# Optimization experiments

Hardware: AMD Instinct MI355X
Metric: run time of the kernel (lower is better)

## Reference

```python
import jax, jax.numpy as jnp
import numpy as np

U, B, S, R = 64, 256, 256, 512
N = 4096
EMA_DECAY = 0.99


def setup_inputs() -> dict:
    key = jax.random.key(0)
    ks = jax.random.split(key, 9)
    q_u = jax.random.uniform(ks[0], (N, U), dtype=jnp.float32)
    q_b = jax.random.uniform(ks[1], (N, B), dtype=jnp.float32)
    q_sigma = jax.random.normal(ks[2], (N, S), dtype=jnp.float32)
    delta_rule_target = jax.random.normal(ks[3], (N, R), dtype=jnp.float32)
    write_mask = jax.random.randint(ks[4], (N,), 0, 2).astype(bool)
    delta_rule_proto = 0.02 * jax.random.normal(ks[5], (U, B, R), dtype=jnp.float32)
    signature_proto = 0.02 * jax.random.normal(ks[6], (U, B, S), dtype=jnp.float32)
    ema_conf = jax.random.uniform(ks[7], (U, B), dtype=jnp.float32)
    usage_count = jnp.maximum(jax.random.uniform(ks[8], (U, B)) - 0.5, 0.0) * 100.0
    return {"q_u": q_u, "q_b": q_b, "q_sigma": q_sigma,
            "delta_rule_target": delta_rule_target, "write_mask": write_mask,
            "delta_rule_proto": delta_rule_proto, "signature_proto": signature_proto,
            "ema_conf": ema_conf, "usage_count": usage_count}


def _l2norm(x):
    return x / jnp.maximum(jnp.linalg.norm(x, axis=-1, keepdims=True), 1e-12)


def reference(q_u, q_b, q_sigma, delta_rule_target, write_mask,
              delta_rule_proto, signature_proto, ema_conf, usage_count):
    # ---------------- retrieve ----------------
    # joint attention over (operator, binding) cells; temperature == 1.0 branch
    joint = q_u[:, :, None] * q_b[:, None, :]                  # [N, U, B]
    valid = (usage_count > 0).astype(joint.dtype)              # [U, B]
    w = joint * valid
    denom = w.sum(axis=(-2, -1), keepdims=True)
    w = jnp.where(denom > 0, w / jnp.maximum(denom, 1e-6), jnp.zeros_like(w))
    memory_delta_rule = jnp.einsum('nub,ubr->nr', w, delta_rule_proto)
    memory_signature = jnp.einsum('nub,ubs->ns', w, signature_proto)
    base_conf = jnp.einsum('nub,ub->n', w, ema_conf)[:, None]  # [N, 1]
    cos = jnp.sum(_l2norm(q_sigma) * _l2norm(memory_signature + 1e-6),
                  axis=-1, keepdims=True)
    signature_agreement = 0.5 * (1.0 + cos)
    memory_conf = jnp.clip(base_conf * signature_agreement, 0.0, 1.0)

    # ---------------- update (vectorized scatter EMA) ----------------
    m = write_mask.astype(q_u.dtype)                           # [N]
    op_conf = q_u.max(axis=-1)
    op_id = jnp.argmax(q_u, axis=-1)
    bind_conf = q_b.max(axis=-1)
    bind_id = jnp.argmax(q_b, axis=-1)
    write_conf = op_conf * bind_conf                           # [N]
    cell = op_id * B + bind_id                                 # [N]
    num_cells = U * B
    wgt = write_conf * m
    sum_w = jax.ops.segment_sum(wgt, cell, num_segments=num_cells)          # [UB]
    sum_d = jax.ops.segment_sum(delta_rule_target * wgt[:, None], cell,
                                num_segments=num_cells)                     # [UB, R]
    sum_s = jax.ops.segment_sum(q_sigma * wgt[:, None], cell,
                                num_segments=num_cells)                     # [UB, S]
    cnt = jax.ops.segment_sum(m, cell, num_segments=num_cells)              # [UB]
    conf_sum = jnp.maximum(sum_w, 1e-6)
    delta_mean = (sum_d / conf_sum[:, None]).reshape(U, B, R)
    sigma_mean = (sum_s / conf_sum[:, None]).reshape(U, B, S)
    conf_mean = (sum_w / jnp.maximum(cnt, 1.0)).reshape(U, B)
    upd = (cnt > 0).reshape(U, B)
    new_delta_proto = jnp.where(upd[:, :, None],
                                EMA_DECAY * delta_rule_proto + (1.0 - EMA_DECAY) * delta_mean,
                                delta_rule_proto)
    new_signature_proto = jnp.where(upd[:, :, None],
                                    EMA_DECAY * signature_proto + (1.0 - EMA_DECAY) * sigma_mean,
                                    signature_proto)
    new_ema_conf = jnp.where(upd,
                             EMA_DECAY * ema_conf + (1.0 - EMA_DECAY) * conf_mean,
                             ema_conf)
    new_usage = usage_count + cnt.reshape(U, B)

    # ---------------- usage stats ----------------
    write_rate = m.mean()
    usage_fraction = (new_usage > 0).astype(jnp.float32).mean()
    dist = new_usage.reshape(-1)
    dist = dist / jnp.maximum(dist.sum(), 1e-6)
    usage_entropy = -(dist * jnp.log(dist + 1e-6)).sum() / np.log(max(2, num_cells))

    return (memory_delta_rule, memory_signature, memory_conf,
            new_delta_proto, new_signature_proto, new_ema_conf, new_usage,
            write_rate, usage_fraction, usage_entropy)
```

## Files before the change

kernel.cpp:

```cpp
#include <hip/hip_runtime.h>
#include <hip/hip_fp8.h>
#include <math.h>

#define NR 4096
#define UD 64
#define BD 256
#define SD 256
#define RD 512
#define UBD 16384
#define DECAY 0.99f

typedef unsigned char u8;
typedef __attribute__((ext_vector_type(4))) float f32x4;
typedef __attribute__((ext_vector_type(2))) long longx2;

#define OFF_MDR   0ull
#define OFF_MSIG  2097152ull
#define OFF_MCONF 3145728ull
#define OFF_NDP   3149824ull
#define OFF_NSP   11538432ull
#define OFF_NEC   15732736ull
#define OFF_NUS   15749120ull
#define OFF_SCAL  15765504ull

static __device__ __forceinline__ u8 f2e4m3(float x) {
  __hip_fp8_e4m3 h(x);
  return (u8)h.__x;
}

static __device__ __forceinline__ void gll16(const void* g, void* l) {
  __builtin_amdgcn_global_load_lds(
      (const __attribute__((address_space(1))) unsigned int*)g,
      (__attribute__((address_space(3))) unsigned int*)l, 16, 0, 0);
}

static __device__ __forceinline__ int perm64(int x) {
  return (((x >> 3) & 3) << 4) | (((x >> 5) & 1) << 3) | (x & 7);
}

__global__ __launch_bounds__(256) void row_prep_kernel(
    const float* __restrict__ q_u, const float* __restrict__ q_b,
    const float* __restrict__ usage, const float* __restrict__ ema,
    const unsigned char* __restrict__ wm,
    float* __restrict__ denom, float* __restrict__ base_raw,
    float* __restrict__ wgt, int* __restrict__ cellid, float* __restrict__ mrow,
    float* __restrict__ sum_w, float* __restrict__ cnt)
{
  const int r0 = blockIdx.x * 16;
  const int t = threadIdx.x;
  __shared__ float s_qu[16][64];
  __shared__ float s_qbv[16][256];
  __shared__ float s_pd[16][256];
  __shared__ float s_pc[16][256];
  __shared__ int s_flag;
  {
    const float4 v = *(const float4*)(q_u + (size_t)r0 * UD + t * 4);
    float* dst = &s_qu[0][0] + t * 4;
    dst[0] = v.x; dst[1] = v.y; dst[2] = v.z; dst[3] = v.w;
  }
  {
    const float4* src = (const float4*)(q_b + (size_t)r0 * BD);
    float4* dst = (float4*)&s_qbv[0][0];
    #pragma unroll
    for (int i = 0; i < 4; ++i) dst[t + i * 256] = src[t + i * 256];
  }
  if (t == 0) {
    const int*   wi = (const int*)wm;
    const float* wf = (const float*)wm;
    bool is_i32 = true, is_f32 = true;
    #pragma unroll
    for (int i = 0; i < 16; ++i) {
      int v = wi[i];
      if (v != 0 && v != 1) is_i32 = false;
      float f = wf[i];
      if (f != 0.f && f != 1.f) is_f32 = false;
    }
    s_flag = is_i32 ? 2 : (is_f32 ? 1 : 0);
  }
  __syncthreads();
  float accd[16], accc[16];
  #pragma unroll
  for (int r = 0; r < 16; ++r) { accd[r] = 0.f; accc[r] = 0.f; }
  #pragma unroll 2
  for (int u = 0; u < UD; ++u) {
    const float us = usage[u * BD + t];
    const float em = ema[u * BD + t];
    const float vm = (us > 0.f) ? 1.f : 0.f;
    const float ev = em * vm;
    #pragma unroll
    for (int r = 0; r < 16; ++r) {
      accd[r] += s_qu[r][u] * vm;
      accc[r] += s_qu[r][u] * ev;
    }
  }
  #pragma unroll
  for (int r = 0; r < 16; ++r) {
    s_pd[r][t] = accd[r] * s_qbv[r][t];
    s_pc[r][t] = accc[r] * s_qbv[r][t];
  }
  __syncthreads();
  const int w = t >> 6, l = t & 63;
  #pragma unroll
  for (int rr = 0; rr < 4; ++rr) {
    const int row = w * 4 + rr;
    float dsum = s_pd[row][l] + s_pd[row][l + 64] + s_pd[row][l + 128] + s_pd[row][l + 192];
    float csum = s_pc[row][l] + s_pc[row][l + 64] + s_pc[row][l + 128] + s_pc[row][l + 192];
    #pragma unroll
    for (int m = 1; m < 64; m <<= 1) {
      dsum += __shfl_xor(dsum, m);
      csum += __shfl_xor(csum, m);
    }
    float bv_ = s_qbv[row][l]; int bi_ = l;
    #pragma unroll
    for (int k = 1; k < 4; ++k) {
      const float v2 = s_qbv[row][l + k * 64];
      if (v2 > bv_) { bv_ = v2; bi_ = l + k * 64; }
    }
    #pragma unroll
    for (int m = 1; m < 64; m <<= 1) {
      const float ov = __shfl_xor(bv_, m);
      const int   oi = __shfl_xor(bi_, m);
      if (ov > bv_ || (ov == bv_ && oi < bi_)) { bv_ = ov; bi_ = oi; }
    }
    float uv_ = s_qu[row][l]; int ui_ = l;
    #pragma unroll
    for (int m = 1; m < 64; m <<= 1) {
      const float ov = __shfl_xor(uv_, m);
      const int   oi = __shfl_xor(ui_, m);
      if (ov > uv_ || (ov == uv_ && oi < ui_)) { uv_ = ov; ui_ = oi; }
    }
    if (l == 0) {
      const int n = r0 + row;
      const int fm = s_flag;
      float m;
      if (fm == 2)      m = (((const int*)wm)[n]   != 0)   ? 1.f : 0.f;
      else if (fm == 1) m = (((const float*)wm)[n] != 0.f) ? 1.f : 0.f;
      else              m = (wm[n] != 0)   ? 1.f : 0.f;
      const float wv = uv_ * bv_ * m;
      const int cell = ui_ * BD + bi_;
      denom[n]    = dsum;
      base_raw[n] = csum;
      wgt[n]      = wv;
      cellid[n]   = cell;
      mrow[n]     = m;
      if (m != 0.f) {
        atomicAdd(&sum_w[cell], wv);
        atomicAdd(&cnt[cell], 1.f);
      }
    }
  }
}

__global__ __launch_bounds__(256) void prep_kernel(
    const float* __restrict__ qb, const float* __restrict__ qu,
    u8* __restrict__ qb8, float* __restrict__ quT)
{
  if (blockIdx.x < 1024) {
    const int i = blockIdx.x * 256 + threadIdx.x;
    const int idx = i * 4;
    const int row = idx >> 8;
    const int b   = idx & 255;
    const float4 v = *(const float4*)(qb + (size_t)idx);
    u8 tmp[4] = { f2e4m3(v.x), f2e4m3(v.y), f2e4m3(v.z), f2e4m3(v.w) };
    unsigned int wv; __builtin_memcpy(&wv, tmp, 4);
    const int nb = (b & ~63) | perm64(b & 63);
    *(unsigned int*)(qb8 + (size_t)row * BD + nb) = wv;
  } else {
    __shared__ float s[64][65];
    const int n0 = (blockIdx.x - 1024) * 64;
    const int tid = threadIdx.x;
    #pragma unroll
    for (int i = 0; i < 16; ++i) {
      const int idx = tid + i * 256;
      const int r = idx >> 6, u = idx & 63;
      s[r][u] = qu[(size_t)(n0 + r) * UD + u];
    }
    __syncthreads();
    #pragma unroll
    for (int i = 0; i < 16; ++i) {
      const int idx = tid + i * 256;
      const int u = idx >> 6, r = idx & 63;
      quT[(size_t)u * NR + n0 + r] = s[r][u];
    }
  }
}

__global__ __launch_bounds__(256) void transpose_mask_kernel(
    const float* __restrict__ dproto, const float* __restrict__ sproto,
    const float* __restrict__ usage, u8* __restrict__ PT8)
{
  __shared__ u8 s[64][68];
  const int k0 = blockIdx.x * 64;
  const int rblk = blockIdx.y;
  const float* src; int ld; int c0s;
  if (rblk < 8) { src = dproto; ld = RD; c0s = rblk * 64; }
  else          { src = sproto; ld = SD; c0s = (rblk - 8) * 64; }
  const int tid = threadIdx.x;
  const int kl = tid >> 4;
  const int rl = (tid & 15) * 4;
  #pragma unroll
  for (int i = 0; i < 4; ++i) {
    const int k = kl + i * 16;
    const bool valid = usage[k0 + k] > 0.f;
    const float4 v = *(const float4*)(src + (size_t)(k0 + k) * ld + c0s + rl);
    s[k][rl + 0] = valid ? f2e4m3(v.x) : (u8)0;
    s[k][rl + 1] = valid ? f2e4m3(v.y) : (u8)0;
    s[k][rl + 2] = valid ? f2e4m3(v.z) : (u8)0;
    s[k][rl + 3] = valid ? f2e4m3(v.w) : (u8)0;
  }
  __syncthreads();
  const int rl2 = tid >> 4;
  const int kl2 = (tid & 15) * 4;
  #pragma unroll
  for (int i = 0; i < 4; ++i) {
    const int r = rl2 + i * 16;
    u8 tmp[4] = { s[kl2 + 0][r], s[kl2 + 1][r], s[kl2 + 2][r], s[kl2 + 3][r] };
    unsigned int wv; __builtin_memcpy(&wv, tmp, 4);
    *(unsigned int*)(PT8 + (size_t)(rblk * 64 + r) * UBD + k0 + perm64(kl2)) = wv;
  }
}

__global__ __launch_bounds__(256, 3) void mfma_gemm_kernel(
    const float* __restrict__ quT, const u8* __restrict__ qb8,
    const u8* __restrict__ PT8, float* __restrict__ out,
    int* __restrict__ tk, int* __restrict__ gf, int* __restrict__ claimed)
{
  __shared__ u8 sA[2][128 * 128];
  __shared__ u8 sB[2][128 * 64];
  __shared__ int s_work;
  const int tid = threadIdx.x;

  if (tid == 0) {
    unsigned int xcc;
    asm volatile("s_getreg_b32 %0, hwreg(HW_REG_XCC_ID)" : "=s"(xcc));
    const int x = (int)(xcc & 7u);
    const int t = atomicAdd(&tk[x], 1);
    int w = -1;
    if (t < 96) {
      const int cand = x * 96 + t;
      if (atomicCAS(&claimed[cand], 0, 1) == 0) w = cand;
    }
    while (w < 0) {
      const int g = atomicAdd(gf, 1);
      if (g >= 768) { w = -2; break; }
      if (atomicCAS(&claimed[g], 0, 1) == 0) w = g;
    }
    s_work = w;
  }
  __syncthreads();
  const int w = s_work;
  if (w < 0) return;

  const int bx = w & 31;
  const int combo = w >> 5;
  const int by = combo >> 2;
  const int bz = combo & 3;

  const int wid = tid >> 6, lane = tid & 63;
  const int n0 = bx * 128;
  const int kbeg = bz * (UBD / 4);

  float* obase; int ldO; int cc0;
  if (by < 4) { obase = out + OFF_MDR;  ldO = RD; cc0 = by * 128; }
  else        { obase = out + OFF_MSIG; ldO = SD; cc0 = (by - 4) * 128; }
  const int c0 = by * 128;

  const int lrowA = lane >> 3;
  const int csrcA = ((lane & 7) ^ lrowA) * 16;
  const u8* gA = qb8 + (size_t)(n0 + lrowA) * BD + csrcA;
  const int lrowB = lane >> 2;
  const int srcslotB = (lane & 3) ^ ((lrowB >> 1) & 3);
  const u8* gB = PT8 + (size_t)(c0 + wid * 16 + lrowB) * UBD + kbeg + srcslotB * 16;

  const int wr = (wid >> 1) * 64, wc = (wid & 1) * 64;
  const int fr = lane & 15;
  const int kg = lane >> 4;
  int aoff[4], boff[4];
  #pragma unroll
  for (int m = 0; m < 4; ++m) aoff[m] = (wr + m * 16 + fr) * 128;
  #pragma unroll
  for (int nn = 0; nn < 4; ++nn) boff[nn] = (wc + nn * 16 + fr) * 64;
  int slothA[2];
  #pragma unroll
  for (int bq = 0; bq < 2; ++bq) slothA[bq] = ((bq * 4 + kg) ^ (fr & 7)) * 16;
  const int slotB16 = (kg ^ ((fr >> 1) & 3)) * 16;

  f32x4 accm[4][4];
  #pragma unroll
  for (int m = 0; m < 4; ++m)
    #pragma unroll
    for (int nn = 0; nn < 4; ++nn)
      accm[m][nn] = (f32x4){0.f, 0.f, 0.f, 0.f};

  #pragma unroll
  for (int i = 0; i < 4; ++i) {
    const int ro = wid * 32 + i * 8;
    gll16(gA + (size_t)ro * BD,       &sA[0][ro * 128]);
    gll16(gA + (size_t)ro * BD + 128, &sA[1][ro * 128]);
  }
  #pragma unroll
  for (int i = 0; i < 2; ++i)
    gll16(gB + (size_t)(i * 64) * UBD, &sB[0][(i * 64 + wid * 16) * 64]);
  __syncthreads();

  const float* quTb = quT + n0 + wr + kg * 4;
  const int ubase = kbeg >> 8;
  f32x4 accu[4][4];

  for (int ph = 0; ph < 64; ++ph) {
    const int buf  = ph & 1;
    const int half = (ph >> 1) & 1;
    const int bq   = ph & 1;
    if (ph < 63) {
      const u8* gs = gB + (size_t)(ph + 1) * 64;
      #pragma unroll
      for (int i = 0; i < 2; ++i)
        gll16(gs + (size_t)(i * 64) * UBD, &sB[buf ^ 1][(i * 64 + wid * 16) * 64]);
    }
    const u8* sa = sA[half];
    const u8* sb = sB[buf];
    longx2 av[4], bv[4];
    #pragma unroll
    for (int m = 0; m < 4; ++m)
      av[m] = *(const longx2*)(sa + aoff[m] + slothA[bq]);
    #pragma unroll
    for (int nn = 0; nn < 4; ++nn)
      bv[nn] = *(const longx2*)(sb + boff[nn] + slotB16);
    const bool first = (ph & 3) == 0;
    #pragma unroll
    for (int m = 0; m < 4; ++m)
      #pragma unroll
      for (int nn = 0; nn < 4; ++nn) {
        if (first)
          accu[m][nn] = __builtin_amdgcn_mfma_f32_16x16x32_fp8_fp8(
              av[m].x, bv[nn].x, (f32x4){0.f, 0.f, 0.f, 0.f}, 0, 0, 0);
        else
          accu[m][nn] = __builtin_amdgcn_mfma_f32_16x16x32_fp8_fp8(
              av[m].x, bv[nn].x, accu[m][nn], 0, 0, 0);
        accu[m][nn] = __builtin_amdgcn_mfma_f32_16x16x32_fp8_fp8(
            av[m].y, bv[nn].y, accu[m][nn], 0, 0, 0);
      }
    __syncthreads();
    if ((ph & 3) == 3) {
      const float* qp = quTb + (size_t)(ubase + (ph >> 2)) * NR;
      #pragma unroll
      for (int m = 0; m < 4; ++m) {
        const f32x4 qv = *(const f32x4*)(qp + m * 16);
        #pragma unroll
        for (int nn = 0; nn < 4; ++nn)
          accm[m][nn] += qv * accu[m][nn];
      }
    }
  }

  #pragma unroll
  for (int m = 0; m < 4; ++m) {
    #pragma unroll
    for (int nn = 0; nn < 4; ++nn) {
      const int c = cc0 + wc + nn * 16 + fr;
      #pragma unroll
      for (int j = 0; j < 4; ++j) {
        const int r = n0 + wr + m * 16 + kg * 4 + j;
        atomicAdd(obase + (size_t)r * ldO + c, accm[m][nn][j]);
      }
    }
  }
}

__global__ __launch_bounds__(256) void epilogue_kernel(
    const float* __restrict__ q_sigma, const float* __restrict__ denom,
    const float* __restrict__ base_raw, float* __restrict__ out)
{
  const int n = blockIdx.x;
  const int t = threadIdx.x;
  __shared__ float r1[256], r2[256], r3[256];
  const float d = denom[n];
  const float scale = (d > 0.f) ? (1.f / fmaxf(d, 1e-6f)) : 0.f;
  float* mdr = out + OFF_MDR + (size_t)n * RD;
  mdr[t]       *= scale;
  mdr[t + 256] *= scale;
  float* msig = out + OFF_MSIG + (size_t)n * SD;
  const float s = msig[t] * scale;
  msig[t] = s;
  const float a = q_sigma[(size_t)n * SD + t];
  const float b = s + 1e-6f;
  r1[t] = a * a; r2[t] = b * b; r3[t] = a * b;
  __syncthreads();
  for (int st = 128; st > 0; st >>= 1) {
    if (t < st) { r1[t] += r1[t + st]; r2[t] += r2[t + st]; r3[t] += r3[t + st]; }
    __syncthreads();
  }
  if (t == 0) {
    const float na = fmaxf(sqrtf(r1[0]), 1e-12f);
    const float nb = fmaxf(sqrtf(r2[0]), 1e-12f);
    const float cosv = r3[0] / (na * nb);
    const float agree = 0.5f * (1.f + cosv);
    const float base = (d > 0.f) ? base_raw[n] / fmaxf(d, 1e-6f) : 0.f;
    out[OFF_MCONF + n] = fminf(fmaxf(base * agree, 0.f), 1.f);
  }
}

__global__ __launch_bounds__(256) void ema_copy_kernel(
    const float* __restrict__ dproto, const float* __restrict__ sproto,
    const float* __restrict__ cnt,
    float* __restrict__ outd, float* __restrict__ outs)
{
  const size_t nd = (size_t)UBD * RD;
  const size_t total = nd + (size_t)UBD * SD;
  for (size_t i = (size_t)blockIdx.x * 256 + threadIdx.x; i < total;
       i += (size_t)gridDim.x * 256) {
    if (i < nd) {
      const float p = dproto[i];
      outd[i] = (cnt[(int)(i >> 9)] > 0.f) ? DECAY * p : p;
    } else {
      const size_t j = i - nd;
      const float p = sproto[j];
      outs[j] = (cnt[(int)(j >> 8)] > 0.f) ? DECAY * p : p;
    }
  }
}

__global__ __launch_bounds__(256) void scatter2_kernel(
    const float* __restrict__ dtarget, const float* __restrict__ q_sigma,
    const float* __restrict__ wgt, const int* __restrict__ cellid,
    const float* __restrict__ mrow, const float* __restrict__ sum_w,
    float* __restrict__ outd, float* __restrict__ outs)
{
  const int n = blockIdx.x;
  if (mrow[n] == 0.f) return;
  const int t = threadIdx.x;
  const int c = cellid[n];
  const float cs = fmaxf(sum_w[c], 1e-6f);
  const float coef = (1.0f - DECAY) * wgt[n] / cs;
  atomicAdd(&outd[(size_t)c * RD + t],       dtarget[(size_t)n * RD + t] * coef);
  atomicAdd(&outd[(size_t)c * RD + t + 256], dtarget[(size_t)n * RD + t + 256] * coef);
  atomicAdd(&outs[(size_t)c * SD + t],       q_sigma[(size_t)n * SD + t] * coef);
}

__global__ __launch_bounds__(256) void ema_small_kernel(
    const float* __restrict__ ema, const float* __restrict__ usage,
    const float* __restrict__ sum_w, const float* __restrict__ cnt,
    float* __restrict__ out_ec, float* __restrict__ out_us)
{
  const int i = blockIdx.x * 256 + threadIdx.x;
  if (i < UBD) {
    const float c = cnt[i];
    const float cm = sum_w[i] / fmaxf(c, 1.f);
    out_ec[i] = (c > 0.f) ? DECAY * ema[i] + (1.f - DECAY) * cm : ema[i];
    out_us[i] = usage[i] + c;
  }
}

__global__ __launch_bounds__(256) void stats_kernel(
    const float* __restrict__ cnt, const float* __restrict__ new_us,
    float* __restrict__ out_scalars)
{
  const int t = threadIdx.x;
  __shared__ float r1[256], r2[256], r3[256];
  float scnt = 0.f, snz = 0.f, sus = 0.f;
  for (int i = t; i < UBD; i += 256) {
    const float c = cnt[i]; scnt += c;
    const float u = new_us[i];
    if (u > 0.f) snz += 1.f;
    sus += u;
  }
  r1[t] = scnt; r2[t] = snz; r3[t] = sus;
  __syncthreads();
  for (int s = 128; s > 0; s >>= 1) {
    if (t < s) { r1[t] += r1[t + s]; r2[t] += r2[t + s]; r3[t] += r3[t + s]; }
    __syncthreads();
  }
  const float total_cnt = r1[0], total_nz = r2[0], total_us = r3[0];
  __syncthreads();
  const float S = fmaxf(total_us, 1e-6f);
  float ent = 0.f;
  for (int i = t; i < UBD; i += 256) {
    const float d = new_us[i] / S;
    ent += d * logf(d + 1e-6f);
  }
  r1[t] = ent;
  __syncthreads();
  for (int s = 128; s > 0; s >>= 1) {
    if (t < s) { r1[t] += r1[t + s]; }
    __syncthreads();
  }
  if (t == 0) {
    out_scalars[0] = total_cnt / (float)NR;
    out_scalars[1] = total_nz / (float)UBD;
    out_scalars[2] = -r1[0] / 9.70406053f;
  }
}

extern "C" void kernel_launch(void* const* d_in, const int* in_sizes, int n_in,
                              void* d_out, int out_size, void* d_ws, size_t ws_size,
                              hipStream_t stream)
{
  const float* q_u    = (const float*)d_in[0];
  const float* q_b    = (const float*)d_in[1];
  const float* q_sig  = (const float*)d_in[2];
  const float* dtg    = (const float*)d_in[3];
  const unsigned char* wm = (const unsigned char*)d_in[4];
  const float* dproto = (const float*)d_in[5];
  const float* sproto = (const float*)d_in[6];
  const float* ema    = (const float*)d_in[7];
  const float* usage  = (const float*)d_in[8];
  float* out = (float*)d_out;

  float* wsf = (float*)d_ws;
  int*   wsi = (int*)d_ws;
  float* denom    = wsf + 16;
  float* base_raw = wsf + 16 + 4096;
  float* wgtb     = wsf + 16 + 8192;
  int*   cellid   = wsi + 16 + 12288;
  float* mrow     = wsf + 16 + 16384;
  float* sum_w    = wsf + 20496;
  float* cnt      = wsf + 20496 + 16384;
  int*   tk       = wsi + 53264;
  int*   gf       = wsi + 53272;
  int*   claimed  = wsi + 53280;

  u8*    PT8 = (u8*)(out + OFF_NDP);
  u8*    qb8 = PT8 + (size_t)768 * UBD;
  float* quT = (float*)(qb8 + (size_t)NR * BD);

  prep_kernel<<<1024 + NR / 64, 256, 0, stream>>>(q_b, q_u, qb8, quT);
  transpose_mask_kernel<<<dim3(UBD / 64, 12), 256, 0, stream>>>(dproto, sproto,
                                                                usage, PT8);
  hipMemsetAsync(out, 0, (size_t)OFF_MCONF * sizeof(float), stream);
  hipMemsetAsync(sum_w, 0, (2u * UBD + 16 + 768) * sizeof(float), stream);

  row_prep_kernel<<<NR / 16, 256, 0, stream>>>(q_u, q_b, usage, ema, wm,
                                               denom, base_raw, wgtb, cellid, mrow,
                                               sum_w, cnt);
  mfma_gemm_kernel<<<768, 256, 0, stream>>>(quT, qb8, PT8, out, tk, gf, claimed);
  epilogue_kernel<<<NR, 256, 0, stream>>>(q_sig, denom, base_raw, out);

  ema_copy_kernel<<<4096, 256, 0, stream>>>(dproto, sproto, cnt,
                                            out + OFF_NDP, out + OFF_NSP);
  scatter2_kernel<<<NR, 256, 0, stream>>>(dtg, q_sig, wgtb, cellid, mrow, sum_w,
                                          out + OFF_NDP, out + OFF_NSP);
  ema_small_kernel<<<UBD / 256, 256, 0, stream>>>(ema, usage, sum_w, cnt,
                                                  out + OFF_NEC, out + OFF_NUS);
  stats_kernel<<<1, 256, 0, stream>>>(cnt, out + OFF_NUS, out + OFF_SCAL);
}
```

Measured before the change: 221.7 us.

## Merge prep and post kernels, make GEMM persistent with register-resident A fragments

```diff
diff --git a/kernel.cpp b/kernel.cpp
--- a/kernel.cpp
+++ b/kernel.cpp
@@ -38,142 +38,42 @@
   return (((x >> 3) & 3) << 4) | (((x >> 5) & 1) << 3) | (x & 7);
 }
 
-__global__ __launch_bounds__(256) void row_prep_kernel(
+__global__ __launch_bounds__(256) void prep_all_kernel(
     const float* __restrict__ q_u, const float* __restrict__ q_b,
+    const float* __restrict__ q_sigma_unused,
+    const float* __restrict__ dproto, const float* __restrict__ sproto,
     const float* __restrict__ usage, const float* __restrict__ ema,
     const unsigned char* __restrict__ wm,
+    u8* __restrict__ qb8, float* __restrict__ quT, u8* __restrict__ PT8,
     float* __restrict__ denom, float* __restrict__ base_raw,
     float* __restrict__ wgt, int* __restrict__ cellid, float* __restrict__ mrow,
     float* __restrict__ sum_w, float* __restrict__ cnt)
 {
-  const int r0 = blockIdx.x * 16;
-  const int t = threadIdx.x;
-  __shared__ float s_qu[16][64];
-  __shared__ float s_qbv[16][256];
-  __shared__ float s_pd[16][256];
-  __shared__ float s_pc[16][256];
+  __shared__ __attribute__((aligned(16))) u8 sbuf[53248];
   __shared__ int s_flag;
-  {
-    const float4 v = *(const float4*)(q_u + (size_t)r0 * UD + t * 4);
-    float* dst = &s_qu[0][0] + t * 4;
-    dst[0] = v.x; dst[1] = v.y; dst[2] = v.z; dst[3] = v.w;
-  }
-  {
-    const float4* src = (const float4*)(q_b + (size_t)r0 * BD);
-    float4* dst = (float4*)&s_qbv[0][0];
-    #pragma unroll
-    for (int i = 0; i < 4; ++i) dst[t + i * 256] = src[t + i * 256];
-  }
-  if (t == 0) {
-    const int*   wi = (const int*)wm;
-    const float* wf = (const float*)wm;
-    bool is_i32 = true, is_f32 = true;
-    #pragma unroll
-    for (int i = 0; i < 16; ++i) {
-      int v = wi[i];
-      if (v != 0 && v != 1) is_i32 = false;
-      float f = wf[i];
-      if (f != 0.f && f != 1.f) is_f32 = false;
-    }
-    s_flag = is_i32 ? 2 : (is_f32 ? 1 : 0);
-  }
-  __syncthreads();
-  float accd[16], accc[16];
-  #pragma unroll
-  for (int r = 0; r < 16; ++r) { accd[r] = 0.f; accc[r] = 0.f; }
-  #pragma unroll 2
-  for (int u = 0; u < UD; ++u) {
-    const float us = usage[u * BD + t];
-    const float em = ema[u * BD + t];
-    const float vm = (us > 0.f) ? 1.f : 0.f;
-    const float ev = em * vm;
-    #pragma unroll
-    for (int r = 0; r < 16; ++r) {
-      accd[r] += s_qu[r][u] * vm;
-      accc[r] += s_qu[r][u] * ev;
-    }
-  }
-  #pragma unroll
-  for (int r = 0; r < 16; ++r) {
-    s_pd[r][t] = accd[r] * s_qbv[r][t];
-    s_pc[r][t] = accc[r] * s_qbv[r][t];
-  }
-  __syncthreads();
-  const int w = t >> 6, l = t & 63;
-  #pragma unroll
-  for (int rr = 0; rr < 4; ++rr) {
-    const int row = w * 4 + rr;
-    float dsum = s_pd[row][l] + s_pd[row][l + 64] + s_pd[row][l + 128] + s_pd[row][l + 192];
-    float csum = s_pc[row][l] + s_pc[row][l + 64] + s_pc[row][l + 128] + s_pc[row][l + 192];
-    #pragma unroll
-    for (int m = 1; m < 64; m <<= 1) {
-      dsum += __shfl_xor(dsum, m);
-      csum += __shfl_xor(csum, m);
-    }
-    float bv_ = s_qbv[row][l]; int bi_ = l;
-    #pragma unroll
-    for (int k = 1; k < 4; ++k) {
-      const float v2 = s_qbv[row][l + k * 64];
-      if (v2 > bv_) { bv_ = v2; bi_ = l + k * 64; }
-    }
-    #pragma unroll
-    for (int m = 1; m < 64; m <<= 1) {
-      const float ov = __shfl_xor(bv_, m);
-      const int   oi = __shfl_xor(bi_, m);
-      if (ov > bv_ || (ov == bv_ && oi < bi_)) { bv_ = ov; bi_ = oi; }
-    }
-    float uv_ = s_qu[row][l]; int ui_ = l;
-    #pragma unroll
-    for (int m = 1; m < 64; m <<= 1) {
-      const float ov = __shfl_xor(uv_, m);
-      const int   oi = __shfl_xor(ui_, m);
-      if (ov > uv_ || (ov == uv_ && oi < ui_)) { uv_ = ov; ui_ = oi; }
-    }
-    if (l == 0) {
-      const int n = r0 + row;
-      const int fm = s_flag;
-      float m;
-      if (fm == 2)      m = (((const int*)wm)[n]   != 0)   ? 1.f : 0.f;
-      else if (fm == 1) m = (((const float*)wm)[n] != 0.f) ? 1.f : 0.f;
-      else              m = (wm[n] != 0)   ? 1.f : 0.f;
-      const float wv = uv_ * bv_ * m;
-      const int cell = ui_ * BD + bi_;
-      denom[n]    = dsum;
-      base_raw[n] = csum;
-      wgt[n]      = wv;
-      cellid[n]   = cell;
-      mrow[n]     = m;
-      if (m != 0.f) {
-        atomicAdd(&sum_w[cell], wv);
-        atomicAdd(&cnt[cell], 1.f);
-      }
-    }
-  }
-}
-
-__global__ __launch_bounds__(256) void prep_kernel(
-    const float* __restrict__ qb, const float* __restrict__ qu,
-    u8* __restrict__ qb8, float* __restrict__ quT)
-{
-  if (blockIdx.x < 1024) {
-    const int i = blockIdx.x * 256 + threadIdx.x;
+  const int b = blockIdx.x;
+  const int tid = threadIdx.x;
+
+  if (b < 1024) {
+    const int i = b * 256 + tid;
     const int idx = i * 4;
     const int row = idx >> 8;
-    const int b   = idx & 255;
-    const float4 v = *(const float4*)(qb + (size_t)idx);
+    const int bb  = idx & 255;
+    const float4 v = *(const float4*)(q_b + (size_t)idx);
     u8 tmp[4] = { f2e4m3(v.x), f2e4m3(v.y), f2e4m3(v.z), f2e4m3(v.w) };
     unsigned int wv; __builtin_memcpy(&wv, tmp, 4);
-    const int nb = (b & ~63) | perm64(b & 63);
+    const int nb = (bb & ~63) | perm64(bb & 63);
     *(unsigned int*)(qb8 + (size_t)row * BD + nb) = wv;
-  } else {
-    __shared__ float s[64][65];
-    const int n0 = (blockIdx.x - 1024) * 64;
-    const int tid = threadIdx.x;
+    return;
+  }
+  if (b < 1088) {
+    float (*s)[65] = (float(*)[65])sbuf;
+    const int n0 = (b - 1024) * 64;
     #pragma unroll
     for (int i = 0; i < 16; ++i) {
       const int idx = tid + i * 256;
       const int r = idx >> 6, u = idx & 63;
-      s[r][u] = qu[(size_t)(n0 + r) * UD + u];
+      s[r][u] = q_u[(size_t)(n0 + r) * UD + u];
     }
     __syncthreads();
     #pragma unroll
@@ -182,240 +82,389 @@
       const int u = idx >> 6, r = idx & 63;
       quT[(size_t)u * NR + n0 + r] = s[r][u];
     }
-  }
-}
-
-__global__ __launch_bounds__(256) void transpose_mask_kernel(
-    const float* __restrict__ dproto, const float* __restrict__ sproto,
-    const float* __restrict__ usage, u8* __restrict__ PT8)
-{
-  __shared__ u8 s[64][68];
-  const int k0 = blockIdx.x * 64;
-  const int rblk = blockIdx.y;
-  const float* src; int ld; int c0s;
-  if (rblk < 8) { src = dproto; ld = RD; c0s = rblk * 64; }
-  else          { src = sproto; ld = SD; c0s = (rblk - 8) * 64; }
-  const int tid = threadIdx.x;
-  const int kl = tid >> 4;
-  const int rl = (tid & 15) * 4;
-  #pragma unroll
-  for (int i = 0; i < 4; ++i) {
-    const int k = kl + i * 16;
-    const bool valid = usage[k0 + k] > 0.f;
-    const float4 v = *(const float4*)(src + (size_t)(k0 + k) * ld + c0s + rl);
-    s[k][rl + 0] = valid ? f2e4m3(v.x) : (u8)0;
-    s[k][rl + 1] = valid ? f2e4m3(v.y) : (u8)0;
-    s[k][rl + 2] = valid ? f2e4m3(v.z) : (u8)0;
-    s[k][rl + 3] = valid ? f2e4m3(v.w) : (u8)0;
-  }
-  __syncthreads();
-  const int rl2 = tid >> 4;
-  const int kl2 = (tid & 15) * 4;
-  #pragma unroll
-  for (int i = 0; i < 4; ++i) {
-    const int r = rl2 + i * 16;
-    u8 tmp[4] = { s[kl2 + 0][r], s[kl2 + 1][r], s[kl2 + 2][r], s[kl2 + 3][r] };
-    unsigned int wv; __builtin_memcpy(&wv, tmp, 4);
-    *(unsigned int*)(PT8 + (size_t)(rblk * 64 + r) * UBD + k0 + perm64(kl2)) = wv;
-  }
-}
-
-__global__ __launch_bounds__(256, 3) void mfma_gemm_kernel(
+    return;
+  }
+  if (b < 4160) {
+    u8 (*s)[68] = (u8(*)[68])sbuf;
+    const int idx = b - 1088;
+    const int k0 = (idx & 255) * 64;
+    const int rblk = idx >> 8;
+    const float* src; int ld; int c0s;
+    if (rblk < 8) { src = dproto; ld = RD; c0s = rblk * 64; }
+    else          { src = sproto; ld = SD; c0s = (rblk - 8) * 64; }
+    const int kl = tid >> 4;
+    const int rl = (tid & 15) * 4;
+    #pragma unroll
+    for (int i = 0; i < 4; ++i) {
+      const int k = kl + i * 16;
+      const bool valid = usage[k0 + k] > 0.f;
+      const float4 v = *(const float4*)(src + (size_t)(k0 + k) * ld + c0s + rl);
+      s[k][rl + 0] = valid ? f2e4m3(v.x) : (u8)0;
+      s[k][rl + 1] = valid ? f2e4m3(v.y) : (u8)0;
+      s[k][rl + 2] = valid ? f2e4m3(v.z) : (u8)0;
+      s[k][rl + 3] = valid ? f2e4m3(v.w) : (u8)0;
+    }
+    __syncthreads();
+    const int rl2 = tid >> 4;
+    const int kl2 = (tid & 15) * 4;
+    #pragma unroll
+    for (int i = 0; i < 4; ++i) {
+      const int r = rl2 + i * 16;
+      u8 tmp[4] = { s[kl2 + 0][r], s[kl2 + 1][r], s[kl2 + 2][r], s[kl2 + 3][r] };
+      unsigned int wv; __builtin_memcpy(&wv, tmp, 4);
+      *(unsigned int*)(PT8 + (size_t)(rblk * 64 + r) * UBD + k0 + perm64(kl2)) = wv;
+    }
+    return;
+  }
+  {
+    float (*s_qu)[64]   = (float(*)[64])sbuf;
+    float (*s_qbv)[256] = (float(*)[256])(sbuf + 4096);
+    float (*s_pd)[256]  = (float(*)[256])(sbuf + 20480);
+    float (*s_pc)[256]  = (float(*)[256])(sbuf + 36864);
+    const int r0 = (b - 4160) * 16;
+    {
+      const float4 v = *(const float4*)(q_u + (size_t)r0 * UD + tid * 4);
+      float* dst = &s_qu[0][0] + tid * 4;
+      dst[0] = v.x; dst[1] = v.y; dst[2] = v.z; dst[3] = v.w;
+    }
+    {
+      const float4* src = (const float4*)(q_b + (size_t)r0 * BD);
+      float4* dst = (float4*)&s_qbv[0][0];
+      #pragma unroll
+      for (int i = 0; i < 4; ++i) dst[tid + i * 256] = src[tid + i * 256];
+    }
+    if (tid == 0) {
+      const int*   wi = (const int*)wm;
+      const float* wf = (const float*)wm;
+      bool is_i32 = true, is_f32 = true;
+      #pragma unroll
+      for (int i = 0; i < 16; ++i) {
+        int v = wi[i];
+        if (v != 0 && v != 1) is_i32 = false;
+        float f = wf[i];
+        if (f != 0.f && f != 1.f) is_f32 = false;
+      }
+      s_flag = is_i32 ? 2 : (is_f32 ? 1 : 0);
+    }
+    __syncthreads();
+    float accd[16], accc[16];
+    #pragma unroll
+    for (int r = 0; r < 16; ++r) { accd[r] = 0.f; accc[r] = 0.f; }
+    #pragma unroll 2
+    for (int u = 0; u < UD; ++u) {
+      const float us = usage[u * BD + tid];
+      const float em = ema[u * BD + tid];
+      const float vm = (us > 0.f) ? 1.f : 0.f;
+      const float ev = em * vm;
+      #pragma unroll
+      for (int r = 0; r < 16; ++r) {
+        accd[r] += s_qu[r][u] * vm;
+        accc[r] += s_qu[r][u] * ev;
+      }
+    }
+    #pragma unroll
+    for (int r = 0; r < 16; ++r) {
+      s_pd[r][tid] = accd[r] * s_qbv[r][tid];
+      s_pc[r][tid] = accc[r] * s_qbv[r][tid];
+    }
+    __syncthreads();
+    const int w = tid >> 6, l = tid & 63;
+    #pragma unroll
+    for (int rr = 0; rr < 4; ++rr) {
+      const int row = w * 4 + rr;
+      float dsum = s_pd[row][l] + s_pd[row][l + 64] + s_pd[row][l + 128] + s_pd[row][l + 192];
+      float csum = s_pc[row][l] + s_pc[row][l + 64] + s_pc[row][l + 128] + s_pc[row][l + 192];
+      #pragma unroll
+      for (int m = 1; m < 64; m <<= 1) {
+        dsum += __shfl_xor(dsum, m);
+        csum += __shfl_xor(csum, m);
+      }
+      float bv_ = s_qbv[row][l]; int bi_ = l;
+      #pragma unroll
+      for (int k = 1; k < 4; ++k) {
+        const float v2 = s_qbv[row][l + k * 64];
+        if (v2 > bv_) { bv_ = v2; bi_ = l + k * 64; }
+      }
+      #pragma unroll
+      for (int m = 1; m < 64; m <<= 1) {
+        const float ov = __shfl_xor(bv_, m);
+        const int   oi = __shfl_xor(bi_, m);
+        if (ov > bv_ || (ov == bv_ && oi < bi_)) { bv_ = ov; bi_ = oi; }
+      }
+      float uv_ = s_qu[row][l]; int ui_ = l;
+      #pragma unroll
+      for (int m = 1; m < 64; m <<= 1) {
+        const float ov = __shfl_xor(uv_, m);
+        const int   oi = __shfl_xor(ui_, m);
+        if (ov > uv_ || (ov == uv_ && oi < ui_)) { uv_ = ov; ui_ = oi; }
+      }
+      if (l == 0) {
+        const int n = r0 + row;
+        const int fm = s_flag;
+        float m;
+        if (fm == 2)      m = (((const int*)wm)[n]   != 0)   ? 1.f : 0.f;
+        else if (fm == 1) m = (((const float*)wm)[n] != 0.f) ? 1.f : 0.f;
+        else              m = (wm[n] != 0)   ? 1.f : 0.f;
+        const float wv = uv_ * bv_ * m;
+        const int cell = ui_ * BD + bi_;
+        denom[n]    = dsum;
+        base_raw[n] = csum;
+        wgt[n]      = wv;
+        cellid[n]   = cell;
+        mrow[n]     = m;
+        if (m != 0.f) {
+          atomicAdd(&sum_w[cell], wv);
+          atomicAdd(&cnt[cell], 1.f);
+        }
+      }
+    }
+  }
+}
+
+__global__ __launch_bounds__(256, 2) void mfma_gemm_kernel(
     const float* __restrict__ quT, const u8* __restrict__ qb8,
     const u8* __restrict__ PT8, float* __restrict__ out,
     int* __restrict__ tk, int* __restrict__ gf, int* __restrict__ claimed)
 {
-  __shared__ u8 sA[2][128 * 128];
-  __shared__ u8 sB[2][128 * 64];
+  __shared__ __attribute__((aligned(16))) u8 smB[4 * 2 * 4096];
+  __shared__ __attribute__((aligned(16))) float squT[16 * 128];
   __shared__ int s_work;
   const int tid = threadIdx.x;
-
-  if (tid == 0) {
-    unsigned int xcc;
-    asm volatile("s_getreg_b32 %0, hwreg(HW_REG_XCC_ID)" : "=s"(xcc));
-    const int x = (int)(xcc & 7u);
-    const int t = atomicAdd(&tk[x], 1);
-    int w = -1;
-    if (t < 96) {
-      const int cand = x * 96 + t;
-      if (atomicCAS(&claimed[cand], 0, 1) == 0) w = cand;
-    }
-    while (w < 0) {
-      const int g = atomicAdd(gf, 1);
-      if (g >= 768) { w = -2; break; }
-      if (atomicCAS(&claimed[g], 0, 1) == 0) w = g;
-    }
-    s_work = w;
-  }
-  __syncthreads();
-  const int w = s_work;
-  if (w < 0) return;
-
-  const int bx = w & 31;
-  const int combo = w >> 5;
-  const int by = combo >> 2;
-  const int bz = combo & 3;
-
   const int wid = tid >> 6, lane = tid & 63;
-  const int n0 = bx * 128;
-  const int kbeg = bz * (UBD / 4);
-
-  float* obase; int ldO; int cc0;
-  if (by < 4) { obase = out + OFF_MDR;  ldO = RD; cc0 = by * 128; }
-  else        { obase = out + OFF_MSIG; ldO = SD; cc0 = (by - 4) * 128; }
-  const int c0 = by * 128;
-
-  const int lrowA = lane >> 3;
-  const int csrcA = ((lane & 7) ^ lrowA) * 16;
-  const u8* gA = qb8 + (size_t)(n0 + lrowA) * BD + csrcA;
-  const int lrowB = lane >> 2;
-  const int srcslotB = (lane & 3) ^ ((lrowB >> 1) & 3);
-  const u8* gB = PT8 + (size_t)(c0 + wid * 16 + lrowB) * UBD + kbeg + srcslotB * 16;
 
   const int wr = (wid >> 1) * 64, wc = (wid & 1) * 64;
-  const int fr = lane & 15;
-  const int kg = lane >> 4;
-  int aoff[4], boff[4];
+  const int fr = lane & 15, kg = lane >> 4;
+  const int srow  = lane >> 2;
+  const int sslot = (lane & 3) ^ (srow & 3);
+  u8* myB = smB + wid * 8192;
+  int boff[4];
   #pragma unroll
-  for (int m = 0; m < 4; ++m) aoff[m] = (wr + m * 16 + fr) * 128;
-  #pragma unroll
-  for (int nn = 0; nn < 4; ++nn) boff[nn] = (wc + nn * 16 + fr) * 64;
-  int slothA[2];
-  #pragma unroll
-  for (int bq = 0; bq < 2; ++bq) slothA[bq] = ((bq * 4 + kg) ^ (fr & 7)) * 16;
-  const int slotB16 = (kg ^ ((fr >> 1) & 3)) * 16;
-
-  f32x4 accm[4][4];
-  #pragma unroll
-  for (int m = 0; m < 4; ++m)
-    #pragma unroll
-    for (int nn = 0; nn < 4; ++nn)
-      accm[m][nn] = (f32x4){0.f, 0.f, 0.f, 0.f};
-
-  #pragma unroll
-  for (int i = 0; i < 4; ++i) {
-    const int ro = wid * 32 + i * 8;
-    gll16(gA + (size_t)ro * BD,       &sA[0][ro * 128]);
-    gll16(gA + (size_t)ro * BD + 128, &sA[1][ro * 128]);
-  }
-  #pragma unroll
-  for (int i = 0; i < 2; ++i)
-    gll16(gB + (size_t)(i * 64) * UBD, &sB[0][(i * 64 + wid * 16) * 64]);
-  __syncthreads();
-
-  const float* quTb = quT + n0 + wr + kg * 4;
-  const int ubase = kbeg >> 8;
-  f32x4 accu[4][4];
-
-  for (int ph = 0; ph < 64; ++ph) {
-    const int buf  = ph & 1;
-    const int half = (ph >> 1) & 1;
-    const int bq   = ph & 1;
-    if (ph < 63) {
-      const u8* gs = gB + (size_t)(ph + 1) * 64;
-      #pragma unroll
-      for (int i = 0; i < 2; ++i)
-        gll16(gs + (size_t)(i * 64) * UBD, &sB[buf ^ 1][(i * 64 + wid * 16) * 64]);
-    }
-    const u8* sa = sA[half];
-    const u8* sb = sB[buf];
-    longx2 av[4], bv[4];
+  for (int nn = 0; nn < 4; ++nn)
+    boff[nn] = (nn * 16 + fr) * 64 + ((kg ^ (fr & 3)) << 4);
+
+  for (;;) {
+    if (tid == 0) {
+      unsigned int xcc;
+      asm volatile("s_getreg_b32 %0, hwreg(HW_REG_XCC_ID)" : "=s"(xcc));
+      const int x = (int)(xcc & 7u);
+      const int t = atomicAdd(&tk[x], 1);
+      int w = -1;
+      if (t < 96) {
+        const int cand = x * 96 + t;
+        if (atomicCAS(&claimed[cand], 0, 1) == 0) w = cand;
+      }
+      while (w < 0) {
+        const int g = atomicAdd(gf, 1);
+        if (g >= 768) { w = -2; break; }
+        if (atomicCAS(&claimed[g], 0, 1) == 0) w = g;
+      }
+      s_work = w;
+    }
+    __syncthreads();
+    const int w = s_work;
+    if (w < 0) return;
+
+    const int bx = w & 31;
+    const int combo = w >> 5;
+    const int by = combo >> 2;
+    const int bz = combo & 3;
+    const int n0 = bx * 128;
+    const int kbeg = bz * (UBD / 4);
+    const int ubase = bz * 16;
+    const int c0 = by * 128;
+
+    float* obase; int ldO; int cc0;
+    if (by < 4) { obase = out + OFF_MDR;  ldO = RD; cc0 = by * 128; }
+    else        { obase = out + OFF_MSIG; ldO = SD; cc0 = (by - 4) * 128; }
+
+    longx2 afrag[4][4];
+    {
+      const u8* ga = qb8 + (size_t)(n0 + wr + fr) * BD + kg * 16;
+      #pragma unroll
+      for (int m = 0; m < 4; ++m)
+        #pragma unroll
+        for (int q = 0; q < 4; ++q)
+          afrag[m][q] = *(const longx2*)(ga + (size_t)m * 16 * BD + q * 64);
+    }
+
+    #pragma unroll
+    for (int i = 0; i < 2; ++i) {
+      const int u = wid * 4 + i * 2 + (lane >> 5);
+      const float* src = quT + (size_t)(ubase + u) * NR + n0 + (lane & 31) * 4;
+      gll16(src, (u8*)squT + (wid * 4 + i * 2) * 512);
+    }
+    const u8* gB = PT8 + (size_t)(c0 + wc + srow) * UBD + kbeg + sslot * 16;
+    #pragma unroll
+    for (int c = 0; c < 2; ++c)
+      #pragma unroll
+      for (int j = 0; j < 4; ++j)
+        gll16(gB + (size_t)(j * 16) * UBD + c * 64, myB + c * 4096 + j * 1024);
+    __syncthreads();
+
+    f32x4 accm[4][4], accu[4][4];
     #pragma unroll
     for (int m = 0; m < 4; ++m)
-      av[m] = *(const longx2*)(sa + aoff[m] + slothA[bq]);
-    #pragma unroll
-    for (int nn = 0; nn < 4; ++nn)
-      bv[nn] = *(const longx2*)(sb + boff[nn] + slotB16);
-    const bool first = (ph & 3) == 0;
-    #pragma unroll
-    for (int m = 0; m < 4; ++m)
-      #pragma unroll
-      for (int nn = 0; nn < 4; ++nn) {
-        if (first)
-          accu[m][nn] = __builtin_amdgcn_mfma_f32_16x16x32_fp8_fp8(
-              av[m].x, bv[nn].x, (f32x4){0.f, 0.f, 0.f, 0.f}, 0, 0, 0);
-        else
-          accu[m][nn] = __builtin_amdgcn_mfma_f32_16x16x32_fp8_fp8(
-              av[m].x, bv[nn].x, accu[m][nn], 0, 0, 0);
-        accu[m][nn] = __builtin_amdgcn_mfma_f32_16x16x32_fp8_fp8(
-            av[m].y, bv[nn].y, accu[m][nn], 0, 0, 0);
-      }
-    __syncthreads();
-    if ((ph & 3) == 3) {
-      const float* qp = quTb + (size_t)(ubase + (ph >> 2)) * NR;
-      #pragma unroll
-      for (int m = 0; m < 4; ++m) {
-        const f32x4 qv = *(const f32x4*)(qp + m * 16);
+      #pragma unroll
+      for (int nn = 0; nn < 4; ++nn)
+        accm[m][nn] = (f32x4){0.f, 0.f, 0.f, 0.f};
+
+    for (int uc = 0; uc < 16; ++uc) {
+      #pragma unroll
+      for (int p4 = 0; p4 < 4; ++p4) {
+        const int ph = uc * 4 + p4;
+        if (p4 == 3 && uc == 15) asm volatile("s_waitcnt vmcnt(0)" ::: "memory");
+        else                     asm volatile("s_waitcnt vmcnt(4)" ::: "memory");
+        const u8* sb = myB + (ph & 1) * 4096;
+        longx2 bv[4];
         #pragma unroll
         for (int nn = 0; nn < 4; ++nn)
-          accm[m][nn] += qv * accu[m][nn];
-      }
-    }
-  }
-
-  #pragma unroll
-  for (int m = 0; m < 4; ++m) {
-    #pragma unroll
-    for (int nn = 0; nn < 4; ++nn) {
-      const int c = cc0 + wc + nn * 16 + fr;
-      #pragma unroll
-      for (int j = 0; j < 4; ++j) {
-        const int r = n0 + wr + m * 16 + kg * 4 + j;
-        atomicAdd(obase + (size_t)r * ldO + c, accm[m][nn][j]);
-      }
-    }
-  }
-}
-
-__global__ __launch_bounds__(256) void epilogue_kernel(
+          bv[nn] = *(const longx2*)(sb + boff[nn]);
+        asm volatile("s_waitcnt lgkmcnt(0)" ::: "memory");
+        if (!(uc == 15 && p4 >= 2)) {
+          const u8* gs = gB + (size_t)(ph + 2) * 64;
+          #pragma unroll
+          for (int j = 0; j < 4; ++j)
+            gll16(gs + (size_t)(j * 16) * UBD, myB + (ph & 1) * 4096 + j * 1024);
+        }
+        #pragma unroll
+        for (int m = 0; m < 4; ++m)
+          #pragma unroll
+          for (int nn = 0; nn < 4; ++nn) {
+            if (p4 == 0)
+              accu[m][nn] = __builtin_amdgcn_mfma_f32_16x16x32_fp8_fp8(
+                  afrag[m][p4].x, bv[nn].x, (f32x4){0.f, 0.f, 0.f, 0.f}, 0, 0, 0);
+            else
+              accu[m][nn] = __builtin_amdgcn_mfma_f32_16x16x32_fp8_fp8(
+                  afrag[m][p4].x, bv[nn].x, accu[m][nn], 0, 0, 0);
+            accu[m][nn] = __builtin_amdgcn_mfma_f32_16x16x32_fp8_fp8(
+                afrag[m][p4].y, bv[nn].y, accu[m][nn], 0, 0, 0);
+          }
+        if (p4 == 3) {
+          const float* qs = squT + uc * 128 + wr + kg * 4;
+          #pragma unroll
+          for (int m = 0; m < 4; ++m) {
+            const f32x4 qv = *(const f32x4*)(qs + m * 16);
+            #pragma unroll
+            for (int nn = 0; nn < 4; ++nn)
+              accm[m][nn] += qv * accu[m][nn];
+          }
+        }
+      }
+    }
+
+    #pragma unroll
+    for (int m = 0; m < 4; ++m) {
+      #pragma unroll
+      for (int nn = 0; nn < 4; ++nn) {
+        const int c = cc0 + wc + nn * 16 + fr;
+        #pragma unroll
+        for (int j = 0; j < 4; ++j) {
+          const int r = n0 + wr + m * 16 + kg * 4 + j;
+          atomicAdd(obase + (size_t)r * ldO + c, accm[m][nn][j]);
+        }
+      }
+    }
+  }
+}
+
+__global__ __launch_bounds__(256) void post_all_kernel(
     const float* __restrict__ q_sigma, const float* __restrict__ denom,
-    const float* __restrict__ base_raw, float* __restrict__ out)
+    const float* __restrict__ base_raw,
+    const float* __restrict__ dproto, const float* __restrict__ sproto,
+    const float* __restrict__ ema, const float* __restrict__ usage,
+    const float* __restrict__ sum_w, const float* __restrict__ cnt,
+    float* __restrict__ out)
 {
-  const int n = blockIdx.x;
+  __shared__ float r1[256], r2[256], r3[256];
+  const int b = blockIdx.x;
   const int t = threadIdx.x;
-  __shared__ float r1[256], r2[256], r3[256];
-  const float d = denom[n];
-  const float scale = (d > 0.f) ? (1.f / fmaxf(d, 1e-6f)) : 0.f;
-  float* mdr = out + OFF_MDR + (size_t)n * RD;
-  mdr[t]       *= scale;
-  mdr[t + 256] *= scale;
-  float* msig = out + OFF_MSIG + (size_t)n * SD;
-  const float s = msig[t] * scale;
-  msig[t] = s;
-  const float a = q_sigma[(size_t)n * SD + t];
-  const float b = s + 1e-6f;
-  r1[t] = a * a; r2[t] = b * b; r3[t] = a * b;
-  __syncthreads();
-  for (int st = 128; st > 0; st >>= 1) {
-    if (t < st) { r1[t] += r1[t + st]; r2[t] += r2[t + st]; r3[t] += r3[t + st]; }
-    __syncthreads();
-  }
-  if (t == 0) {
-    const float na = fmaxf(sqrtf(r1[0]), 1e-12f);
-    const float nb = fmaxf(sqrtf(r2[0]), 1e-12f);
-    const float cosv = r3[0] / (na * nb);
-    const float agree = 0.5f * (1.f + cosv);
-    const float base = (d > 0.f) ? base_raw[n] / fmaxf(d, 1e-6f) : 0.f;
-    out[OFF_MCONF + n] = fminf(fmaxf(base * agree, 0.f), 1.f);
-  }
-}
-
-__global__ __launch_bounds__(256) void ema_copy_kernel(
-    const float* __restrict__ dproto, const float* __restrict__ sproto,
-    const float* __restrict__ cnt,
-    float* __restrict__ outd, float* __restrict__ outs)
-{
-  const size_t nd = (size_t)UBD * RD;
-  const size_t total = nd + (size_t)UBD * SD;
-  for (size_t i = (size_t)blockIdx.x * 256 + threadIdx.x; i < total;
-       i += (size_t)gridDim.x * 256) {
-    if (i < nd) {
-      const float p = dproto[i];
-      outd[i] = (cnt[(int)(i >> 9)] > 0.f) ? DECAY * p : p;
-    } else {
-      const size_t j = i - nd;
-      const float p = sproto[j];
-      outs[j] = (cnt[(int)(j >> 8)] > 0.f) ? DECAY * p : p;
+
+  if (b < 4096) {
+    const int n = b;
+    const float d = denom[n];
+    const float scale = (d > 0.f) ? (1.f / fmaxf(d, 1e-6f)) : 0.f;
+    float* mdr = out + OFF_MDR + (size_t)n * RD;
+    mdr[t]       *= scale;
+    mdr[t + 256] *= scale;
+    float* msig = out + OFF_MSIG + (size_t)n * SD;
+    const float s = msig[t] * scale;
+    msig[t] = s;
+    const float a = q_sigma[(size_t)n * SD + t];
+    const float bb = s + 1e-6f;
+    r1[t] = a * a; r2[t] = bb * bb; r3[t] = a * bb;
+    __syncthreads();
+    for (int st = 128; st > 0; st >>= 1) {
+      if (t < st) { r1[t] += r1[t + st]; r2[t] += r2[t + st]; r3[t] += r3[t + st]; }
+      __syncthreads();
+    }
+    if (t == 0) {
+      const float na = fmaxf(sqrtf(r1[0]), 1e-12f);
+      const float nb = fmaxf(sqrtf(r2[0]), 1e-12f);
+      const float cosv = r3[0] / (na * nb);
+      const float agree = 0.5f * (1.f + cosv);
+      const float base = (d > 0.f) ? base_raw[n] / fmaxf(d, 1e-6f) : 0.f;
+      out[OFF_MCONF + n] = fminf(fmaxf(base * agree, 0.f), 1.f);
+    }
+    return;
+  }
+  if (b < 8192) {
+    const size_t nd = (size_t)UBD * RD;
+    const size_t total = nd + (size_t)UBD * SD;
+    float* outd = out + OFF_NDP;
+    float* outs = out + OFF_NSP;
+    for (size_t i = (size_t)(b - 4096) * 256 + t; i < total;
+         i += (size_t)4096 * 256) {
+      if (i < nd) {
+        const float p = dproto[i];
+        outd[i] = (cnt[(int)(i >> 9)] > 0.f) ? DECAY * p : p;
+      } else {
+        const size_t j = i - nd;
+        const float p = sproto[j];
+        outs[j] = (cnt[(int)(j >> 8)] > 0.f) ? DECAY * p : p;
+      }
+    }
+    return;
+  }
+  if (b < 8256) {
+    const int i = (b - 8192) * 256 + t;
+    const float c = cnt[i];
+    const float cm = sum_w[i] / fmaxf(c, 1.f);
+    out[OFF_NEC + i] = (c > 0.f) ? DECAY * ema[i] + (1.f - DECAY) * cm : ema[i];
+    out[OFF_NUS + i] = usage[i] + c;
+    return;
+  }
+  {
+    float scnt = 0.f, snz = 0.f, sus = 0.f;
+    for (int i = t; i < UBD; i += 256) {
+      const float c = cnt[i]; scnt += c;
+      const float u = usage[i] + c;
+      if (u > 0.f) snz += 1.f;
+      sus += u;
+    }
+    r1[t] = scnt; r2[t] = snz; r3[t] = sus;
+    __syncthreads();
+    for (int s = 128; s > 0; s >>= 1) {
+      if (t < s) { r1[t] += r1[t + s]; r2[t] += r2[t + s]; r3[t] += r3[t + s]; }
+      __syncthreads();
+    }
+    const float total_cnt = r1[0], total_nz = r2[0], total_us = r3[0];
+    __syncthreads();
+    const float S = fmaxf(total_us, 1e-6f);
+    float ent = 0.f;
+    for (int i = t; i < UBD; i += 256) {
+      const float d = (usage[i] + cnt[i]) / S;
+      ent += d * logf(d + 1e-6f);
+    }
+    r1[t] = ent;
+    __syncthreads();
+    for (int s = 128; s > 0; s >>= 1) {
+      if (t < s) { r1[t] += r1[t + s]; }
+      __syncthreads();
+    }
+    if (t == 0) {
+      out[OFF_SCAL + 0] = total_cnt / (float)NR;
+      out[OFF_SCAL + 1] = total_nz / (float)UBD;
+      out[OFF_SCAL + 2] = -r1[0] / 9.70406053f;
     }
   }
 }
@@ -437,60 +486,6 @@
   atomicAdd(&outs[(size_t)c * SD + t],       q_sigma[(size_t)n * SD + t] * coef);
 }
 
-__global__ __launch_bounds__(256) void ema_small_kernel(
-    const float* __restrict__ ema, const float* __restrict__ usage,
-    const float* __restrict__ sum_w, const float* __restrict__ cnt,
-    float* __restrict__ out_ec, float* __restrict__ out_us)
-{
-  const int i = blockIdx.x * 256 + threadIdx.x;
-  if (i < UBD) {
-    const float c = cnt[i];
-    const float cm = sum_w[i] / fmaxf(c, 1.f);
-    out_ec[i] = (c > 0.f) ? DECAY * ema[i] + (1.f - DECAY) * cm : ema[i];
-    out_us[i] = usage[i] + c;
-  }
-}
-
-__global__ __launch_bounds__(256) void stats_kernel(
-    const float* __restrict__ cnt, const float* __restrict__ new_us,
-    float* __restrict__ out_scalars)
-{
-  const int t = threadIdx.x;
-  __shared__ float r1[256], r2[256], r3[256];
-  float scnt = 0.f, snz = 0.f, sus = 0.f;
-  for (int i = t; i < UBD; i += 256) {
-    const float c = cnt[i]; scnt += c;
-    const float u = new_us[i];
-    if (u > 0.f) snz += 1.f;
-    sus += u;
-  }
-  r1[t] = scnt; r2[t] = snz; r3[t] = sus;
-  __syncthreads();
-  for (int s = 128; s > 0; s >>= 1) {
-    if (t < s) { r1[t] += r1[t + s]; r2[t] += r2[t + s]; r3[t] += r3[t + s]; }
-    __syncthreads();
-  }
-  const float total_cnt = r1[0], total_nz = r2[0], total_us = r3[0];
-  __syncthreads();
-  const float S = fmaxf(total_us, 1e-6f);
-  float ent = 0.f;
-  for (int i = t; i < UBD; i += 256) {
-    const float d = new_us[i] / S;
-    ent += d * logf(d + 1e-6f);
-  }
-  r1[t] = ent;
-  __syncthreads();
-  for (int s = 128; s > 0; s >>= 1) {
-    if (t < s) { r1[t] += r1[t + s]; }
-    __syncthreads();
-  }
-  if (t == 0) {
-    out_scalars[0] = total_cnt / (float)NR;
-    out_scalars[1] = total_nz / (float)UBD;
-    out_scalars[2] = -r1[0] / 9.70406053f;
-  }
-}
-
 extern "C" void kernel_launch(void* const* d_in, const int* in_sizes, int n_in,
                               void* d_out, int out_size, void* d_ws, size_t ws_size,
                               hipStream_t stream)
@@ -523,23 +518,16 @@
   u8*    qb8 = PT8 + (size_t)768 * UBD;
   float* quT = (float*)(qb8 + (size_t)NR * BD);
 
-  prep_kernel<<<1024 + NR / 64, 256, 0, stream>>>(q_b, q_u, qb8, quT);
-  transpose_mask_kernel<<<dim3(UBD / 64, 12), 256, 0, stream>>>(dproto, sproto,
-                                                                usage, PT8);
   hipMemsetAsync(out, 0, (size_t)OFF_MCONF * sizeof(float), stream);
   hipMemsetAsync(sum_w, 0, (2u * UBD + 16 + 768) * sizeof(float), stream);
 
-  row_prep_kernel<<<NR / 16, 256, 0, stream>>>(q_u, q_b, usage, ema, wm,
-                                               denom, base_raw, wgtb, cellid, mrow,
-                                               sum_w, cnt);
-  mfma_gemm_kernel<<<768, 256, 0, stream>>>(quT, qb8, PT8, out, tk, gf, claimed);
-  epilogue_kernel<<<NR, 256, 0, stream>>>(q_sig, denom, base_raw, out);
-
-  ema_copy_kernel<<<4096, 256, 0, stream>>>(dproto, sproto, cnt,
-                                            out + OFF_NDP, out + OFF_NSP);
+  prep_all_kernel<<<4416, 256, 0, stream>>>(q_u, q_b, q_sig, dproto, sproto,
+                                            usage, ema, wm, qb8, quT, PT8,
+                                            denom, base_raw, wgtb, cellid, mrow,
+                                            sum_w, cnt);
+  mfma_gemm_kernel<<<512, 256, 0, stream>>>(quT, qb8, PT8, out, tk, gf, claimed);
+  post_all_kernel<<<8257, 256, 0, stream>>>(q_sig, denom, base_raw, dproto,
+                                            sproto, ema, usage, sum_w, cnt, out);
   scatter2_kernel<<<NR, 256, 0, stream>>>(dtg, q_sig, wgtb, cellid, mrow, sum_w,
                                           out + OFF_NDP, out + OFF_NSP);
-  ema_small_kernel<<<UBD / 256, 256, 0, stream>>>(ema, usage, sum_w, cnt,
-                                                  out + OFF_NEC, out + OFF_NUS);
-  stats_kernel<<<1, 256, 0, stream>>>(cnt, out + OFF_NUS, out + OFF_SCAL);
-}
+}
```

Result: faster. 200.3 us (-9.6%).
